# Kernel optimization log

Hardware: AMD Instinct MI355X
Metric: run time of the kernel (lower is better)

## Reference

```python
import jax, jax.numpy as jnp
import numpy as np
from jax import lax

BN_EPS = 1e-5


def setup_inputs() -> dict:
    key = jax.random.key(0)
    ks = jax.random.split(key, 4)
    T, N, I, H, O, K = 2048, 16, 1024, 2048, 1024, 12
    return {
        "inputs": jax.random.normal(ks[0], (T, N, I), dtype=jnp.float32),
        "wv": jax.random.normal(ks[1], (H, I), dtype=jnp.float32) * (1.0 / np.sqrt(I)),
        "gamma": jnp.ones((H,), dtype=jnp.float32),
        "beta": jnp.zeros((H,), dtype=jnp.float32),
        "wu": jax.random.normal(ks[2], (O, H), dtype=jnp.float32) * (1.0 / np.sqrt(H)),
        "bu": jnp.zeros((O,), dtype=jnp.float32),
        "memory_weights": jax.random.normal(ks[3], (K, H), dtype=jnp.float32) * 0.05,
        "stride": 2,
        "l_memory_size": 10,
        "r_memory_size": 1,
    }


def _memory_block(p, memory_weights, stride, l_mem, r_mem):
    # p: [N, T, H]. p_hatt[n,t,h] = sum_k w[k,h] * p[n, t + (k-l_mem)*stride, h]
    # == depthwise 1D cross-correlation with dilation=stride, 'same' asymmetric pad.
    H = p.shape[-1]
    x = jnp.transpose(p, (0, 2, 1))              # [N, H, T]
    kern = memory_weights.T[:, None, :]          # [H, 1, K]
    out = lax.conv_general_dilated(
        x, kern,
        window_strides=(1,),
        padding=[(l_mem * stride, r_mem * stride)],
        rhs_dilation=(stride,),
        dimension_numbers=("NCH", "OIH", "NCH"),
        feature_group_count=H,
    )
    return jnp.transpose(out, (0, 2, 1))         # [N, T, H]


def reference(inputs, wv, gamma, beta, wu, bu, memory_weights,
              stride, l_memory_size, r_memory_size):
    # wx_v then transpose(0,1): [T,N,I] -> [N,T,H]
    p = jnp.einsum("tni,hi->nth", inputs, wv)
    p_hatt = p + _memory_block(p, memory_weights, stride, l_memory_size, r_memory_size)
    # SequenceWise(BatchNorm1d) in train mode: stats over flattened (N*T) rows.
    H = p_hatt.shape[-1]
    flat = p_hatt.reshape(-1, H)
    mean = flat.mean(axis=0)
    var = flat.var(axis=0)  # biased, matches torch BN normalization
    xn = (p_hatt - mean) * lax.rsqrt(var + BN_EPS) * gamma + beta
    h = jax.nn.relu(jnp.einsum("nth,oh->nto", xn, wu) + bu)
    return (h, p_hatt)
```

## Files before the change

kernel.cpp:

```cpp
#include <hip/hip_runtime.h>
#include <hip/hip_bf16.h>
#include <stdint.h>

#define T_DIM 2048
#define N_DIM 16
#define I_DIM 1024
#define H_DIM 2048
#define O_DIM 1024
#define K_TAPS 12
#define MROWS (N_DIM * T_DIM)
#define BN_EPS 1e-5f

#define S_LEN 1024
#define TCHUNK 48
#define SCHUNKS 22

typedef __attribute__((ext_vector_type(8))) short bf16x8;
typedef __attribute__((ext_vector_type(4))) float f32x4;

__device__ __forceinline__ unsigned short f2bf_rne(float f) {
    union { float f; unsigned u; } v; v.f = f;
    unsigned u = v.u;
    unsigned r = u + 0x7fffu + ((u >> 16) & 1u);
    return (unsigned short)(r >> 16);
}

__device__ __forceinline__ float bf2f(unsigned short x) {
    union { unsigned u; float f; } v; v.u = ((unsigned)x) << 16; return v.f;
}

__global__ void cvt_kernel(const float* __restrict__ in, unsigned short* __restrict__ out, int n4) {
    int i = blockIdx.x * blockDim.x + threadIdx.x;
    int stride = gridDim.x * blockDim.x;
    for (; i < n4; i += stride) {
        float4 v = ((const float4*)in)[i];
        ushort4 o;
        o.x = f2bf_rne(v.x); o.y = f2bf_rne(v.y);
        o.z = f2bf_rne(v.z); o.w = f2bf_rne(v.w);
        ((ushort4*)out)[i] = o;
    }
}

__device__ __forceinline__ void gload_lds16(const void* g, void* l) {
    __builtin_amdgcn_global_load_lds(
        (const __attribute__((address_space(1))) unsigned int*)g,
        (__attribute__((address_space(3))) unsigned int*)l, 16, 0, 0);
}

template<int PERM, int EPI, int KD, int NCOLS>
__global__ __launch_bounds__(512, 2) void gemm256(
    const unsigned short* __restrict__ A,
    const unsigned short* __restrict__ B,
    void* __restrict__ Cout,
    const float* __restrict__ bias)
{
    __shared__ char lds[131072];

    const int tid  = threadIdx.x;
    const int wid  = tid >> 6;
    const int lane = tid & 63;
    const int wr   = (wid >> 2) * 128;
    const int wc   = (wid & 3) * 64;
    const int fr   = lane & 15;
    const int fh   = lane >> 4;

    const int nwg = gridDim.x;
    const int lin = blockIdx.x;
    const int tile = (lin & 7) * (nwg >> 3) + (lin >> 3);
    const int ntx = NCOLS / 256;
    const long c0 = (long)(tile % ntx) * 256;
    const long r0 = (long)(tile / ntx) * 256;

    long aBase, aStride;
    if (PERM) {
        const long n0 = r0 / T_DIM;
        const long t0 = r0 % T_DIM;
        aBase = (t0 * N_DIM + n0) * (long)KD;
        aStride = (long)N_DIM * KD;
    } else {
        aBase = r0 * (long)KD;
        aStride = KD;
    }
    const long bBase = c0 * (long)KD;

    auto stage_half = [&](int buf, int mat, int h, int kt) {
        char* mbase = lds + buf * 65536 + mat * 32768 + h * 16384;
#pragma unroll
        for (int j = 0; j < 2; ++j) {
            const int row = h * 128 + j * 64 + (tid >> 3);
            const int g   = (tid & 7) ^ (row & 7);
            long gelem;
            if (mat == 0) gelem = aBase + (long)row * aStride + (long)kt * 64 + g * 8;
            else          gelem = bBase + (long)row * (long)KD + (long)kt * 64 + g * 8;
            gload_lds16((const char*)(mat == 0 ? A : B) + gelem * 2,
                        mbase + j * 8192 + tid * 16);
        }
    };

    auto rdA = [&](int buf, int m, int ks) -> bf16x8 {
        const int row = wr + m * 16 + fr;
        const int blk = ks * 4 + fh;
        return *(const bf16x8*)(lds + buf * 65536 + row * 128 + ((blk ^ (row & 7)) << 4));
    };
    auto rdB = [&](int buf, int n, int ks) -> bf16x8 {
        const int row = wc + n * 16 + fr;
        const int blk = ks * 4 + fh;
        return *(const bf16x8*)(lds + buf * 65536 + 32768 + row * 128 + ((blk ^ (row & 7)) << 4));
    };

    f32x4 acc[8][4] = {};

    stage_half(0, 0, 0, 0); stage_half(0, 0, 1, 0);
    stage_half(0, 1, 0, 0); stage_half(0, 1, 1, 0);

    const int KT  = KD / 64;
    const int KT2 = KT / 2;
    for (int i = 0; i < KT2; ++i) {
        const int tB = 2 * i + 1;
        const bool haveNext = (i + 1 < KT2);
        bf16x8 bfr[4][2];

#pragma unroll
        for (int q = 0; q < 4; ++q) {
            stage_half(1, q >> 1, q & 1, tB);
            bf16x8 af[2][2];
            if (q == 0) {
                asm volatile("s_waitcnt vmcnt(2)" ::: "memory");
                __builtin_amdgcn_s_barrier();
#pragma unroll
                for (int n = 0; n < 4; ++n)
#pragma unroll
                    for (int ks = 0; ks < 2; ++ks) bfr[n][ks] = rdB(0, n, ks);
#pragma unroll
                for (int mm = 0; mm < 2; ++mm)
#pragma unroll
                    for (int ks = 0; ks < 2; ++ks) af[mm][ks] = rdA(0, q * 2 + mm, ks);
            } else {
#pragma unroll
                for (int mm = 0; mm < 2; ++mm)
#pragma unroll
                    for (int ks = 0; ks < 2; ++ks) af[mm][ks] = rdA(0, q * 2 + mm, ks);
                __builtin_amdgcn_s_barrier();
            }
            __builtin_amdgcn_s_setprio(1);
#pragma unroll
            for (int mm = 0; mm < 2; ++mm)
#pragma unroll
                for (int n = 0; n < 4; ++n)
#pragma unroll
                    for (int ks = 0; ks < 2; ++ks)
                        acc[q * 2 + mm][n] = __builtin_amdgcn_mfma_f32_16x16x32_bf16(
                            af[mm][ks], bfr[n][ks], acc[q * 2 + mm][n], 0, 0, 0);
            __builtin_amdgcn_s_setprio(0);
            __builtin_amdgcn_s_barrier();
        }

#pragma unroll
        for (int q = 0; q < 4; ++q) {
            if (haveNext) stage_half(0, q >> 1, q & 1, 2 * i + 2);
            bf16x8 af[2][2];
            if (q == 0) {
                if (haveNext) asm volatile("s_waitcnt vmcnt(2)" ::: "memory");
                else          asm volatile("s_waitcnt vmcnt(0)" ::: "memory");
                __builtin_amdgcn_s_barrier();
#pragma unroll
                for (int n = 0; n < 4; ++n)
#pragma unroll
                    for (int ks = 0; ks < 2; ++ks) bfr[n][ks] = rdB(1, n, ks);
#pragma unroll
                for (int mm = 0; mm < 2; ++mm)
#pragma unroll
                    for (int ks = 0; ks < 2; ++ks) af[mm][ks] = rdA(1, q * 2 + mm, ks);
            } else {
#pragma unroll
                for (int mm = 0; mm < 2; ++mm)
#pragma unroll
                    for (int ks = 0; ks < 2; ++ks) af[mm][ks] = rdA(1, q * 2 + mm, ks);
                __builtin_amdgcn_s_barrier();
            }
            __builtin_amdgcn_s_setprio(1);
#pragma unroll
            for (int mm = 0; mm < 2; ++mm)
#pragma unroll
                for (int n = 0; n < 4; ++n)
#pragma unroll
                    for (int ks = 0; ks < 2; ++ks)
                        acc[q * 2 + mm][n] = __builtin_amdgcn_mfma_f32_16x16x32_bf16(
                            af[mm][ks], bfr[n][ks], acc[q * 2 + mm][n], 0, 0, 0);
            __builtin_amdgcn_s_setprio(0);
            __builtin_amdgcn_s_barrier();
        }
    }

#pragma unroll
    for (int m = 0; m < 8; ++m) {
        const long orow_base = r0 + wr + m * 16 + fh * 4;
#pragma unroll
        for (int n = 0; n < 4; ++n) {
            const long ocol = c0 + wc + n * 16 + fr;
#pragma unroll
            for (int j = 0; j < 4; ++j) {
                const long orow = orow_base + j;
                float vv = acc[m][n][j];
                if (EPI == 0) {
                    ((unsigned short*)Cout)[orow * NCOLS + ocol] = f2bf_rne(vv);
                } else {
                    vv += bias[ocol];
                    vv = vv > 0.f ? vv : 0.f;
                    ((float*)Cout)[orow * NCOLS + ocol] = vv;
                }
            }
        }
    }
}

__global__ __launch_bounds__(256) void conv_bn_v2(
    const unsigned short* __restrict__ p,
    const float* __restrict__ w,
    float* __restrict__ ph_f32,
    unsigned short* __restrict__ ph_b,
    float* __restrict__ sums)
{
    const int tid   = threadIdx.x;
    const int b     = blockIdx.x;
    const int half  = b & 1;
    const int chunk = (b >> 1) % SCHUNKS;
    const int np    = (b >> 1) / SCHUNKS;
    const int par   = np & 1;
    const int n     = np >> 1;
    const int h0    = half * 1024 + tid * 4;

    float wk[12][4];
#pragma unroll
    for (int k = 0; k < 12; ++k) {
        float4 v = *(const float4*)&w[k * H_DIM + h0];
        wk[k][0] = v.x; wk[k][1] = v.y; wk[k][2] = v.z; wk[k][3] = v.w;
    }

    const long b0 = ((long)n * T_DIM + par) * (long)H_DIM + h0;
    const int s0 = chunk * TCHUNK;

    float win[12][4];
#pragma unroll
    for (int j = 0; j < 12; ++j) {
        const int s = s0 + j - 10;
        if (s >= 0 && s < S_LEN) {
            ushort4 v = *(const ushort4*)&p[b0 + (long)s * (2 * H_DIM)];
            win[j][0] = bf2f(v.x); win[j][1] = bf2f(v.y);
            win[j][2] = bf2f(v.z); win[j][3] = bf2f(v.w);
        } else {
            win[j][0] = 0.f; win[j][1] = 0.f; win[j][2] = 0.f; win[j][3] = 0.f;
        }
    }

    float st1[4] = {0.f, 0.f, 0.f, 0.f};
    float st2[4] = {0.f, 0.f, 0.f, 0.f};

    for (int ss = 0; ss < TCHUNK; ss += 12) {
#pragma unroll
        for (int uu = 0; uu < 12; ++uu) {
            const int s = s0 + ss + uu;
            if (s < S_LEN) {
                float out[4];
#pragma unroll
                for (int c = 0; c < 4; ++c) out[c] = win[(uu + 10) % 12][c];
#pragma unroll
                for (int k = 0; k < 12; ++k)
#pragma unroll
                    for (int c = 0; c < 4; ++c)
                        out[c] += wk[k][c] * win[(uu + k) % 12][c];

                const long base = b0 + (long)s * (2 * H_DIM);
                *(float4*)&ph_f32[base] = make_float4(out[0], out[1], out[2], out[3]);
                ushort4 ob;
                ob.x = f2bf_rne(out[0]); ob.y = f2bf_rne(out[1]);
                ob.z = f2bf_rne(out[2]); ob.w = f2bf_rne(out[3]);
                *(ushort4*)&ph_b[base] = ob;
#pragma unroll
                for (int c = 0; c < 4; ++c) { st1[c] += out[c]; st2[c] += out[c] * out[c]; }
            }
            {
                const int sn = s0 + ss + uu + 2;
                if (sn < S_LEN) {
                    ushort4 v = *(const ushort4*)&p[b0 + (long)sn * (2 * H_DIM)];
                    win[uu][0] = bf2f(v.x); win[uu][1] = bf2f(v.y);
                    win[uu][2] = bf2f(v.z); win[uu][3] = bf2f(v.w);
                } else {
                    win[uu][0] = 0.f; win[uu][1] = 0.f; win[uu][2] = 0.f; win[uu][3] = 0.f;
                }
            }
        }
    }

#pragma unroll
    for (int c = 0; c < 4; ++c) {
        atomicAdd(&sums[h0 + c], st1[c]);
        atomicAdd(&sums[H_DIM + h0 + c], st2[c]);
    }
}

__global__ void bn_finalize(const float* __restrict__ sums,
                            const float* __restrict__ gamma,
                            const float* __restrict__ beta,
                            float* __restrict__ sshift) {
    int h = blockIdx.x * blockDim.x + threadIdx.x;
    if (h >= H_DIM) return;
    float mean = sums[h] * (1.f / (float)MROWS);
    float var  = sums[H_DIM + h] * (1.f / (float)MROWS) - mean * mean;
    float s = gamma[h] * rsqrtf(var + BN_EPS);
    sshift[h] = s;
    sshift[H_DIM + h] = beta[h] - mean * s;
}

__global__ void scale_wu(const float* __restrict__ wu,
                         const float* __restrict__ sshift,
                         unsigned short* __restrict__ wu2) {
    int idx = blockIdx.x * blockDim.x + threadIdx.x;
    int stride = gridDim.x * blockDim.x;
    for (; idx < O_DIM * H_DIM; idx += stride) {
        int h = idx & (H_DIM - 1);
        wu2[idx] = f2bf_rne(wu[idx] * sshift[h]);
    }
}

__global__ __launch_bounds__(256) void bias2_kernel(
    const float* __restrict__ wu,
    const float* __restrict__ sshift,
    const float* __restrict__ bu,
    float* __restrict__ bias2) {
    const int o = blockIdx.x;
    float part = 0.f;
    for (int h = threadIdx.x; h < H_DIM; h += 256)
        part += sshift[H_DIM + h] * wu[(long)o * H_DIM + h];
#pragma unroll
    for (int off = 32; off > 0; off >>= 1) part += __shfl_down(part, off, 64);
    __shared__ float red[4];
    const int wv = threadIdx.x >> 6, lane = threadIdx.x & 63;
    if (lane == 0) red[wv] = part;
    __syncthreads();
    if (threadIdx.x == 0) bias2[o] = bu[o] + red[0] + red[1] + red[2] + red[3];
}

extern "C" void kernel_launch(void* const* d_in, const int* in_sizes, int n_in,
                              void* d_out, int out_size, void* d_ws, size_t ws_size,
                              hipStream_t stream) {
    const float* inputs = (const float*)d_in[0];
    const float* wv     = (const float*)d_in[1];
    const float* gamma  = (const float*)d_in[2];
    const float* beta   = (const float*)d_in[3];
    const float* wu     = (const float*)d_in[4];
    const float* bu     = (const float*)d_in[5];
    const float* mw     = (const float*)d_in[6];

    float* out_h  = (float*)d_out;
    float* out_ph = out_h + (size_t)MROWS * O_DIM;

    unsigned short* p_b = (unsigned short*)d_out;

    char* ws = (char*)d_ws;
    unsigned short* ph_b  = (unsigned short*)ws;
    unsigned short* in_b  = (unsigned short*)(ws + 134217728);
    unsigned short* wv_b  = (unsigned short*)(ws + 201326592);
    unsigned short* wu2_b = (unsigned short*)(ws + 205520896);
    float* sums   = (float*)(ws + 209715200);
    float* sshift = (float*)(ws + 209731584);
    float* bias2  = (float*)(ws + 209747968);

    hipMemsetAsync(sums, 0, 2 * H_DIM * sizeof(float), stream);

    cvt_kernel<<<2048, 256, 0, stream>>>(inputs, in_b, (T_DIM * N_DIM * I_DIM) / 4);
    cvt_kernel<<<512, 256, 0, stream>>>(wv, wv_b, (H_DIM * I_DIM) / 4);

    gemm256<1, 0, I_DIM, H_DIM><<<(MROWS / 256) * (H_DIM / 256), 512, 0, stream>>>(
        in_b, wv_b, (void*)p_b, nullptr);

    conv_bn_v2<<<2 * SCHUNKS * 2 * N_DIM, 256, 0, stream>>>(p_b, mw, out_ph, ph_b, sums);

    bn_finalize<<<(H_DIM + 255) / 256, 256, 0, stream>>>(sums, gamma, beta, sshift);
    scale_wu<<<2048, 256, 0, stream>>>(wu, sshift, wu2_b);
    bias2_kernel<<<O_DIM, 256, 0, stream>>>(wu, sshift, bu, bias2);

    gemm256<0, 1, H_DIM, O_DIM><<<(MROWS / 256) * (O_DIM / 256), 512, 0, stream>>>(
        ph_b, wu2_b, (void*)out_h, bias2);
}
```

Baseline: 460.9 us.

## Fuse fp32-to-bf16 conversion of A operand into GEMM staging

The GEMM now loads its A operand directly as fp32 from global memory into registers, converts it to bf16 and writes it to swizzled LDS. This removes the separate conversion pass over the inputs and the extra bf16 copy of p_hatt, so both GEMMs read fp32 sources directly. The cost is twice the global A traffic per tile, more registers for the prefetch buffers, and a register-staged pipeline in place of the async global-to-LDS loads for A.

```diff
diff --git a/kernel.cpp b/kernel.cpp
--- a/kernel.cpp
+++ b/kernel.cpp
@@ -27,6 +27,15 @@
 
 __device__ __forceinline__ float bf2f(unsigned short x) {
     union { unsigned u; float f; } v; v.u = ((unsigned)x) << 16; return v.f;
+}
+
+__device__ __forceinline__ bf16x8 pack8(const float4& a, const float4& b) {
+    bf16x8 v;
+    v[0] = (short)f2bf_rne(a.x); v[1] = (short)f2bf_rne(a.y);
+    v[2] = (short)f2bf_rne(a.z); v[3] = (short)f2bf_rne(a.w);
+    v[4] = (short)f2bf_rne(b.x); v[5] = (short)f2bf_rne(b.y);
+    v[6] = (short)f2bf_rne(b.z); v[7] = (short)f2bf_rne(b.w);
+    return v;
 }
 
 __global__ void cvt_kernel(const float* __restrict__ in, unsigned short* __restrict__ out, int n4) {
@@ -49,7 +58,7 @@
 
 template<int PERM, int EPI, int KD, int NCOLS>
 __global__ __launch_bounds__(512, 2) void gemm256(
-    const unsigned short* __restrict__ A,
+    const float* __restrict__ A,
     const unsigned short* __restrict__ B,
     void* __restrict__ Cout,
     const float* __restrict__ bias)
@@ -83,18 +92,25 @@
     }
     const long bBase = c0 * (long)KD;
 
-    auto stage_half = [&](int buf, int mat, int h, int kt) {
-        char* mbase = lds + buf * 65536 + mat * 32768 + h * 16384;
-#pragma unroll
-        for (int j = 0; j < 2; ++j) {
-            const int row = h * 128 + j * 64 + (tid >> 3);
-            const int g   = (tid & 7) ^ (row & 7);
-            long gelem;
-            if (mat == 0) gelem = aBase + (long)row * aStride + (long)kt * 64 + g * 8;
-            else          gelem = bBase + (long)row * (long)KD + (long)kt * 64 + g * 8;
-            gload_lds16((const char*)(mat == 0 ? A : B) + gelem * 2,
-                        mbase + j * 8192 + tid * 16);
-        }
+    auto stageB = [&](int buf, int si, int kt) {
+        const int row = si * 64 + (tid >> 3);
+        const int g   = (tid & 7) ^ (row & 7);
+        const long gelem = bBase + (long)row * (long)KD + (long)kt * 64 + g * 8;
+        gload_lds16((const char*)B + gelem * 2,
+                    lds + buf * 65536 + 32768 + si * 8192 + tid * 16);
+    };
+
+    auto loadA = [&](float4* dst, int wi, int kt) {
+        const int row = wi * 64 + (tid >> 3);
+        const long base = aBase + (long)row * aStride + (long)kt * 64 + (tid & 7) * 8;
+        dst[0] = *(const float4*)(A + base);
+        dst[1] = *(const float4*)(A + base + 4);
+    };
+    auto writeA = [&](int buf, int wi, const float4* src) {
+        const int row = wi * 64 + (tid >> 3);
+        const int blk = tid & 7;
+        *(bf16x8*)(lds + buf * 65536 + row * 128 + (((blk ^ (row & 7))) << 4)) =
+            pack8(src[0], src[1]);
     };
 
     auto rdA = [&](int buf, int m, int ks) -> bf16x8 {
@@ -109,86 +125,93 @@
     };
 
     f32x4 acc[8][4] = {};
-
-    stage_half(0, 0, 0, 0); stage_half(0, 0, 1, 0);
-    stage_half(0, 1, 0, 0); stage_half(0, 1, 1, 0);
+    float4 aA[8], aB[8];
+
+    stageB(0, 0, 0); stageB(0, 1, 0); stageB(0, 2, 0); stageB(0, 3, 0);
+    loadA(&aA[0], 0, 0); loadA(&aA[2], 1, 0); loadA(&aA[4], 2, 0); loadA(&aA[6], 3, 0);
+    writeA(0, 0, &aA[0]); writeA(0, 1, &aA[2]); writeA(0, 2, &aA[4]); writeA(0, 3, &aA[6]);
+    loadA(&aB[0], 0, 1); loadA(&aB[2], 1, 1); loadA(&aB[4], 2, 1); loadA(&aB[6], 3, 1);
+    asm volatile("s_waitcnt vmcnt(8) lgkmcnt(0)" ::: "memory");
+    __builtin_amdgcn_s_barrier();
 
     const int KT  = KD / 64;
     const int KT2 = KT / 2;
     for (int i = 0; i < KT2; ++i) {
-        const int tB = 2 * i + 1;
         const bool haveNext = (i + 1 < KT2);
-        bf16x8 bfr[4][2];
-
-#pragma unroll
-        for (int q = 0; q < 4; ++q) {
-            stage_half(1, q >> 1, q & 1, tB);
-            bf16x8 af[2][2];
-            if (q == 0) {
-                asm volatile("s_waitcnt vmcnt(2)" ::: "memory");
-                __builtin_amdgcn_s_barrier();
-#pragma unroll
-                for (int n = 0; n < 4; ++n)
-#pragma unroll
-                    for (int ks = 0; ks < 2; ++ks) bfr[n][ks] = rdB(0, n, ks);
+        const int tB1 = 2 * i + 1, tN = 2 * i + 2, tNN = 2 * i + 3;
+
+        {
+            bf16x8 bfr[4][2];
+#pragma unroll
+            for (int q = 0; q < 4; ++q) {
+                writeA(1, q, &aB[2 * q]);
+                if (q == 0) { stageB(1, 0, tB1); stageB(1, 1, tB1); stageB(1, 2, tB1); stageB(1, 3, tB1); }
+                if (haveNext) loadA(&aA[2 * q], q, tN);
+                if (q == 0) {
+#pragma unroll
+                    for (int n = 0; n < 4; ++n)
+#pragma unroll
+                        for (int ks = 0; ks < 2; ++ks) bfr[n][ks] = rdB(0, n, ks);
+                }
+                bf16x8 af[2][2];
 #pragma unroll
                 for (int mm = 0; mm < 2; ++mm)
 #pragma unroll
                     for (int ks = 0; ks < 2; ++ks) af[mm][ks] = rdA(0, q * 2 + mm, ks);
-            } else {
+                __builtin_amdgcn_s_setprio(1);
 #pragma unroll
                 for (int mm = 0; mm < 2; ++mm)
 #pragma unroll
-                    for (int ks = 0; ks < 2; ++ks) af[mm][ks] = rdA(0, q * 2 + mm, ks);
+                    for (int n = 0; n < 4; ++n)
+#pragma unroll
+                        for (int ks = 0; ks < 2; ++ks)
+                            acc[q * 2 + mm][n] = __builtin_amdgcn_mfma_f32_16x16x32_bf16(
+                                af[mm][ks], bfr[n][ks], acc[q * 2 + mm][n], 0, 0, 0);
+                __builtin_amdgcn_s_setprio(0);
+                if (q == 3) {
+                    if (haveNext) asm volatile("s_waitcnt vmcnt(8) lgkmcnt(0)" ::: "memory");
+                    else          asm volatile("s_waitcnt vmcnt(0) lgkmcnt(0)" ::: "memory");
+                }
                 __builtin_amdgcn_s_barrier();
             }
-            __builtin_amdgcn_s_setprio(1);
-#pragma unroll
-            for (int mm = 0; mm < 2; ++mm)
-#pragma unroll
-                for (int n = 0; n < 4; ++n)
-#pragma unroll
-                    for (int ks = 0; ks < 2; ++ks)
-                        acc[q * 2 + mm][n] = __builtin_amdgcn_mfma_f32_16x16x32_bf16(
-                            af[mm][ks], bfr[n][ks], acc[q * 2 + mm][n], 0, 0, 0);
-            __builtin_amdgcn_s_setprio(0);
-            __builtin_amdgcn_s_barrier();
         }
 
-#pragma unroll
-        for (int q = 0; q < 4; ++q) {
-            if (haveNext) stage_half(0, q >> 1, q & 1, 2 * i + 2);
-            bf16x8 af[2][2];
-            if (q == 0) {
-                if (haveNext) asm volatile("s_waitcnt vmcnt(2)" ::: "memory");
-                else          asm volatile("s_waitcnt vmcnt(0)" ::: "memory");
-                __builtin_amdgcn_s_barrier();
-#pragma unroll
-                for (int n = 0; n < 4; ++n)
-#pragma unroll
-                    for (int ks = 0; ks < 2; ++ks) bfr[n][ks] = rdB(1, n, ks);
+        {
+            bf16x8 bfr[4][2];
+#pragma unroll
+            for (int q = 0; q < 4; ++q) {
+                if (haveNext) {
+                    writeA(0, q, &aA[2 * q]);
+                    if (q == 0) { stageB(0, 0, tN); stageB(0, 1, tN); stageB(0, 2, tN); stageB(0, 3, tN); }
+                    loadA(&aB[2 * q], q, tNN);
+                }
+                if (q == 0) {
+#pragma unroll
+                    for (int n = 0; n < 4; ++n)
+#pragma unroll
+                        for (int ks = 0; ks < 2; ++ks) bfr[n][ks] = rdB(1, n, ks);
+                }
+                bf16x8 af[2][2];
 #pragma unroll
                 for (int mm = 0; mm < 2; ++mm)
 #pragma unroll
                     for (int ks = 0; ks < 2; ++ks) af[mm][ks] = rdA(1, q * 2 + mm, ks);
-            } else {
+                __builtin_amdgcn_s_setprio(1);
 #pragma unroll
                 for (int mm = 0; mm < 2; ++mm)
 #pragma unroll
-                    for (int ks = 0; ks < 2; ++ks) af[mm][ks] = rdA(1, q * 2 + mm, ks);
+                    for (int n = 0; n < 4; ++n)
+#pragma unroll
+                        for (int ks = 0; ks < 2; ++ks)
+                            acc[q * 2 + mm][n] = __builtin_amdgcn_mfma_f32_16x16x32_bf16(
+                                af[mm][ks], bfr[n][ks], acc[q * 2 + mm][n], 0, 0, 0);
+                __builtin_amdgcn_s_setprio(0);
+                if (q == 3) {
+                    if (haveNext) asm volatile("s_waitcnt vmcnt(8) lgkmcnt(0)" ::: "memory");
+                    else          asm volatile("s_waitcnt vmcnt(0) lgkmcnt(0)" ::: "memory");
+                }
                 __builtin_amdgcn_s_barrier();
             }
-            __builtin_amdgcn_s_setprio(1);
-#pragma unroll
-            for (int mm = 0; mm < 2; ++mm)
-#pragma unroll
-                for (int n = 0; n < 4; ++n)
-#pragma unroll
-                    for (int ks = 0; ks < 2; ++ks)
-                        acc[q * 2 + mm][n] = __builtin_amdgcn_mfma_f32_16x16x32_bf16(
-                            af[mm][ks], bfr[n][ks], acc[q * 2 + mm][n], 0, 0, 0);
-            __builtin_amdgcn_s_setprio(0);
-            __builtin_amdgcn_s_barrier();
         }
     }
 
@@ -214,11 +237,10 @@
     }
 }
 
-__global__ __launch_bounds__(256) void conv_bn_v2(
+__global__ __launch_bounds__(256) void conv_bn_v3(
     const unsigned short* __restrict__ p,
     const float* __restrict__ w,
     float* __restrict__ ph_f32,
-    unsigned short* __restrict__ ph_b,
     float* __restrict__ sums)
 {
     const int tid   = threadIdx.x;
@@ -272,10 +294,6 @@
 
                 const long base = b0 + (long)s * (2 * H_DIM);
                 *(float4*)&ph_f32[base] = make_float4(out[0], out[1], out[2], out[3]);
-                ushort4 ob;
-                ob.x = f2bf_rne(out[0]); ob.y = f2bf_rne(out[1]);
-                ob.z = f2bf_rne(out[2]); ob.w = f2bf_rne(out[3]);
-                *(ushort4*)&ph_b[base] = ob;
 #pragma unroll
                 for (int c = 0; c < 4; ++c) { st1[c] += out[c]; st2[c] += out[c] * out[c]; }
             }
@@ -358,8 +376,6 @@
     unsigned short* p_b = (unsigned short*)d_out;
 
     char* ws = (char*)d_ws;
-    unsigned short* ph_b  = (unsigned short*)ws;
-    unsigned short* in_b  = (unsigned short*)(ws + 134217728);
     unsigned short* wv_b  = (unsigned short*)(ws + 201326592);
     unsigned short* wu2_b = (unsigned short*)(ws + 205520896);
     float* sums   = (float*)(ws + 209715200);
@@ -368,18 +384,17 @@
 
     hipMemsetAsync(sums, 0, 2 * H_DIM * sizeof(float), stream);
 
-    cvt_kernel<<<2048, 256, 0, stream>>>(inputs, in_b, (T_DIM * N_DIM * I_DIM) / 4);
     cvt_kernel<<<512, 256, 0, stream>>>(wv, wv_b, (H_DIM * I_DIM) / 4);
 
     gemm256<1, 0, I_DIM, H_DIM><<<(MROWS / 256) * (H_DIM / 256), 512, 0, stream>>>(
-        in_b, wv_b, (void*)p_b, nullptr);
-
-    conv_bn_v2<<<2 * SCHUNKS * 2 * N_DIM, 256, 0, stream>>>(p_b, mw, out_ph, ph_b, sums);
+        inputs, wv_b, (void*)p_b, nullptr);
+
+    conv_bn_v3<<<2 * SCHUNKS * 2 * N_DIM, 256, 0, stream>>>(p_b, mw, out_ph, sums);
 
     bn_finalize<<<(H_DIM + 255) / 256, 256, 0, stream>>>(sums, gamma, beta, sshift);
     scale_wu<<<2048, 256, 0, stream>>>(wu, sshift, wu2_b);
     bias2_kernel<<<O_DIM, 256, 0, stream>>>(wu, sshift, bu, bias2);
 
     gemm256<0, 1, H_DIM, O_DIM><<<(MROWS / 256) * (O_DIM / 256), 512, 0, stream>>>(
-        ph_b, wu2_b, (void*)out_h, bias2);
-}
+        out_ph, wu2_b, (void*)out_h, bias2);
+}
```

New measurement: 498.0 us. +8.1%, slower.
